# Kernel tuning notes

Hardware: AMD Instinct MI355X
Metric: run time of the kernel (lower is better)

Reference implementation:

```python
import jax, jax.numpy as jnp
import numpy as np

HEADS = 16

def setup_inputs() -> dict:
    key = jax.random.key(0)
    ks = jax.random.split(key, 8)
    S, B, D = 2048, 2, 1024
    scale = 0.02
    return {
        'query': jax.random.normal(ks[0], (S, B, D), jnp.float32),
        'key':   jax.random.normal(ks[1], (S, B, D), jnp.float32),
        'value': jax.random.normal(ks[2], (S, B, D), jnp.float32),
        'Wq': jax.random.normal(ks[3], (D, D), jnp.float32) * scale,
        'bq': jnp.zeros((D,), jnp.float32),
        'Wk': jax.random.normal(ks[4], (D, D), jnp.float32) * scale,
        'bk': jnp.zeros((D,), jnp.float32),
        'Wv': jax.random.normal(ks[5], (D, D), jnp.float32) * scale,
        'bv': jnp.zeros((D,), jnp.float32),
        'Wo': jax.random.normal(ks[6], (D, D), jnp.float32) * scale,
        'bo': jnp.zeros((D,), jnp.float32),
    }

def reference(query, key, value, Wq, bq, Wk, bk, Wv, bv, Wo, bo):
    S, B, D = query.shape
    h = HEADS
    dk = D // h
    # projections: nn.Linear stores weight [out, in] -> x @ W.T + b
    q = (query @ Wq.T + bq).reshape(S, B, h, dk)
    k = (key   @ Wk.T + bk).reshape(S, B, h, dk)
    v = (value @ Wv.T + bv).reshape(S, B, h, dk)
    # scores: [i, j, b, h]
    scores = jnp.einsum('ibhd,jbhd->ijbh', q, k) / jnp.sqrt(jnp.asarray(dk, q.dtype))
    # original uses nn.Softmax(dim=1) -> softmax over key axis j
    attn = jax.nn.softmax(scores, axis=1)
    x = jnp.einsum('ijbh,jbhd->ibhd', attn, v).reshape(S, B, D)
    return x @ Wo.T + bo
```

## Files before the change

kernel.cpp:

```cpp
#include <hip/hip_runtime.h>
#include <hip/hip_bf16.h>
#include <math.h>

#define S_LEN  2048
#define NBATCH 2
#define DMODEL 1024
#define NHEADS 16
#define HDIM   64
#define MROWS  (S_LEN*NBATCH)
#define NBH    (NBATCH*NHEADS)

#define QSCALE 0.1803368801111f
#define DEFER_THR 11.5f

typedef __attribute__((ext_vector_type(8))) short          bf16x8;
typedef __attribute__((ext_vector_type(4))) float          f32x4;
typedef __attribute__((ext_vector_type(8))) unsigned short u16x8;

__device__ __forceinline__ unsigned short f2bf(float x) {
    union { __hip_bfloat16 h; unsigned short u; } c;
    c.h = __float2bfloat16(x);
    return c.u;
}
__device__ __forceinline__ unsigned int cvtpk_bf16(float lo, float hi) {
    unsigned int r;
    asm("v_cvt_pk_bf16_f32 %0, %1, %2" : "=v"(r) : "v"(lo), "v"(hi));
    return r;
}

__global__ __launch_bounds__(256)
void cvt7(const float* __restrict__ s0, const float* __restrict__ s1,
          const float* __restrict__ s2, const float* __restrict__ s3,
          const float* __restrict__ s4, const float* __restrict__ s5,
          const float* __restrict__ s6,
          unsigned short* __restrict__ d0, unsigned short* __restrict__ d1,
          unsigned short* __restrict__ d2, unsigned short* __restrict__ d3,
          unsigned short* __restrict__ d4, unsigned short* __restrict__ d5,
          unsigned short* __restrict__ d6)
{
    const float* s; unsigned short* d; int n;
    switch (blockIdx.y) {
        case 0: s = s0; d = d0; n = MROWS*DMODEL;  break;
        case 1: s = s1; d = d1; n = MROWS*DMODEL;  break;
        case 2: s = s2; d = d2; n = MROWS*DMODEL;  break;
        case 3: s = s3; d = d3; n = DMODEL*DMODEL; break;
        case 4: s = s4; d = d4; n = DMODEL*DMODEL; break;
        case 5: s = s5; d = d5; n = DMODEL*DMODEL; break;
        default: s = s6; d = d6; n = DMODEL*DMODEL; break;
    }
    int i = (blockIdx.x*256 + threadIdx.x) * 8;
    if (i >= n) return;
    float4 a = *(const float4*)(s + i);
    float4 b = *(const float4*)(s + i + 4);
    u16x8 o;
    o[0] = f2bf(a.x); o[1] = f2bf(a.y); o[2] = f2bf(a.z); o[3] = f2bf(a.w);
    o[4] = f2bf(b.x); o[5] = f2bf(b.y); o[6] = f2bf(b.z); o[7] = f2bf(b.w);
    *(u16x8*)(d + i) = o;
}

#define GBM 128
#define GBK 32

template<int BN_T, bool TRANS>
__device__ __forceinline__ void gemm_core(
    const unsigned short* __restrict__ A,
    const unsigned short* __restrict__ W,
    const float* __restrict__ bias,
    float* __restrict__ Cf, unsigned short* __restrict__ Cb,
    int mode, float scale)
{
    constexpr int FN  = BN_T / 32;
    constexpr int BCW = BN_T / 64;
    __shared__ __align__(16) unsigned short As[GBM*GBK];
    __shared__ __align__(16) unsigned short Bs[BN_T*GBK];

    const int tid = threadIdx.x;
    const int l   = tid & 63;
    const int w   = tid >> 6;
    const int m0  = blockIdx.y * GBM;
    const int n0  = blockIdx.x * BN_T;
    const int wm  = (w >> 1) * 64;
    const int wn  = (w & 1) * (BN_T/2);

    f32x4 acc[4][FN];
    #pragma unroll
    for (int i = 0; i < 4; ++i)
        #pragma unroll
        for (int j = 0; j < FN; ++j)
            acc[i][j] = (f32x4){0.f, 0.f, 0.f, 0.f};

    const int srow = l >> 2;
    const int scol = (l & 3) * 8;

    for (int k0 = 0; k0 < DMODEL; k0 += GBK) {
        #pragma unroll
        for (int i = 0; i < 2; ++i) {
            int c = w*2 + i;
            const unsigned short* ga = A + (size_t)(m0 + c*16 + srow)*DMODEL + k0 + scol;
            __builtin_amdgcn_global_load_lds(
                (const __attribute__((address_space(1))) void*)ga,
                (__attribute__((address_space(3))) void*)(As + c*512), 16, 0, 0);
        }
        #pragma unroll
        for (int i = 0; i < BCW; ++i) {
            int c = w*BCW + i;
            const unsigned short* gb = W + (size_t)(n0 + c*16 + srow)*DMODEL + k0 + scol;
            __builtin_amdgcn_global_load_lds(
                (const __attribute__((address_space(1))) void*)gb,
                (__attribute__((address_space(3))) void*)(Bs + c*512), 16, 0, 0);
        }
        __syncthreads();

        bf16x8 af[4], bfr[FN];
        #pragma unroll
        for (int f = 0; f < 4; ++f)
            af[f]  = *(const bf16x8*)(As + (wm + f*16 + (l & 15))*GBK + (l >> 4)*8);
        #pragma unroll
        for (int f = 0; f < FN; ++f)
            bfr[f] = *(const bf16x8*)(Bs + (wn + f*16 + (l & 15))*GBK + (l >> 4)*8);
        #pragma unroll
        for (int i = 0; i < 4; ++i)
            #pragma unroll
            for (int j = 0; j < FN; ++j)
                acc[i][j] = __builtin_amdgcn_mfma_f32_16x16x32_bf16(af[i], bfr[j], acc[i][j], 0, 0, 0);
        __syncthreads();
    }

    const int col_l = l & 15;
    const int row_l = (l >> 4) * 4;

    if constexpr (TRANS) {
        if (mode == 2) {
            __shared__ __align__(16) unsigned short tileS[64][136];
            #pragma unroll
            for (int ph = 0; ph < 2; ++ph) {
                __syncthreads();
                if ((w >> 1) == ph) {
                    #pragma unroll
                    for (int j = 0; j < FN; ++j) {
                        int c = wn + j*16 + col_l;
                        float bv = bias[n0 + c];
                        #pragma unroll
                        for (int i = 0; i < 4; ++i)
                            #pragma unroll
                            for (int r = 0; r < 4; ++r)
                                tileS[i*16 + row_l + r][c] = f2bf((acc[i][j][r] + bv) * scale);
                    }
                }
                __syncthreads();
                const int sbase = (m0 + ph*64) >> 1;
                #pragma unroll
                for (int it = 0; it < 4; ++it) {
                    int idx = it*256 + tid;
                    int c    = idx >> 3;
                    int bb   = (idx >> 2) & 1;
                    int sl0  = (idx & 3) * 8;
                    int hh   = (n0 + c) >> 6;
                    int dd   = (n0 + c) & 63;
                    u16x8 ov;
                    #pragma unroll
                    for (int k2 = 0; k2 < 8; ++k2)
                        ov[k2] = tileS[2*(sl0 + k2) + bb][c];
                    *(u16x8*)(Cb + ((size_t)(bb*NHEADS + hh)*HDIM + dd)*S_LEN + sbase + sl0) = ov;
                }
            }
            return;
        }
    }

    #pragma unroll
    for (int j = 0; j < FN; ++j) {
        int col = n0 + wn + j*16 + col_l;
        float bv = bias[col];
        #pragma unroll
        for (int i = 0; i < 4; ++i) {
            int mbase = m0 + wm + i*16 + row_l;
            #pragma unroll
            for (int r = 0; r < 4; ++r) {
                int m = mbase + r;
                float vout = (acc[i][j][r] + bv) * scale;
                if (mode == 0) {
                    Cf[(size_t)m*DMODEL + col] = vout;
                } else {
                    int s = m >> 1, b = m & 1;
                    int h = col >> 6, d = col & 63;
                    Cb[((size_t)(b*NHEADS + h)*S_LEN + s)*HDIM + d] = f2bf(vout);
                }
            }
        }
    }
}

__global__ __launch_bounds__(256)
void gemm_qkv(const unsigned short* __restrict__ qb, const unsigned short* __restrict__ kb,
              const unsigned short* __restrict__ vb,
              const unsigned short* __restrict__ Wqb, const float* __restrict__ bq,
              const unsigned short* __restrict__ Wkb, const float* __restrict__ bk,
              const unsigned short* __restrict__ Wvb, const float* __restrict__ bv,
              unsigned short* __restrict__ qp, unsigned short* __restrict__ kp,
              unsigned short* __restrict__ vt)
{
    const int z = blockIdx.z;
    const unsigned short* A = (z==0) ? qb  : (z==1) ? kb  : vb;
    const unsigned short* W = (z==0) ? Wqb : (z==1) ? Wkb : Wvb;
    const float* bias       = (z==0) ? bq  : (z==1) ? bk  : bv;
    unsigned short* C       = (z==0) ? qp  : (z==1) ? kp  : vt;
    int   mode  = (z==2) ? 2 : 1;
    float scale = (z==0) ? QSCALE : 1.0f;
    gemm_core<128, true>(A, W, bias, nullptr, C, mode, scale);
}

__global__ __launch_bounds__(256)
void gemm_out(const unsigned short* __restrict__ A, const unsigned short* __restrict__ W,
              const float* __restrict__ bias, float* __restrict__ C)
{
    gemm_core<64, false>(A, W, bias, C, nullptr, 0, 1.0f);
}

#define QBLK  128
#define KVBLK 64
#define NT    (S_LEN/KVBLK)

__global__ __launch_bounds__(512)
void attn_mfma(const unsigned short* __restrict__ qp, const unsigned short* __restrict__ kp,
               const unsigned short* __restrict__ vt, unsigned short* __restrict__ x)
{
    __shared__ __align__(16) unsigned short Ks[2][KVBLK*HDIM];
    __shared__ __align__(16) unsigned short Vs[2][KVBLK*HDIM];
    __shared__ __align__(16) unsigned short Ps[8][16*KVBLK];

    const int tid = threadIdx.x;
    const int w   = tid >> 6;
    const int l   = tid & 63;
    const int g   = l >> 4;
    const int s16 = l & 15;
    const int q0  = blockIdx.x * QBLK;
    const int bh  = blockIdx.y;
    const int b   = bh >> 4;
    const int h   = bh & 15;
    const size_t base = (size_t)bh * S_LEN * HDIM;

    char* PsB = (char*)&Ps[w][0];

#define STAGE(buf_, kt_) do {                                                        \
    int row_ = tid >> 3;                                                             \
    int u_   = (tid & 7) ^ (row_ & 7);                                               \
    const unsigned short* gk_ = kp + base + (size_t)((kt_) + row_)*HDIM + u_*8;      \
    __builtin_amdgcn_global_load_lds(                                                \
        (const __attribute__((address_space(1))) void*)gk_,                          \
        (__attribute__((address_space(3))) void*)(Ks[buf_] + w*512), 16, 0, 0);      \
    const unsigned short* gv_ = vt + base + (size_t)row_*S_LEN + (kt_) + u_*8;       \
    __builtin_amdgcn_global_load_lds(                                                \
        (const __attribute__((address_space(1))) void*)gv_,                          \
        (__attribute__((address_space(3))) void*)(Vs[buf_] + w*512), 16, 0, 0);      \
} while (0)

#define ITER(buf_, t_) do {                                                          \
    __syncthreads();                                                                 \
    if ((t_) + 1 < NT) STAGE(buf_ ^ 1, ((t_) + 1)*KVBLK);                            \
    const char* KsB_ = (const char*)Ks[buf_];                                        \
    const char* VsB_ = (const char*)Vs[buf_];                                        \
    f32x4 sacc[4];                                                                   \
    _Pragma("unroll")                                                                \
    for (int mi = 0; mi < 4; ++mi) sacc[mi] = (f32x4){0.f, 0.f, 0.f, 0.f};           \
    __builtin_amdgcn_s_setprio(1);                                                   \
    _Pragma("unroll")                                                                \
    for (int ks = 0; ks < 2; ++ks) {                                                 \
        bf16x8 af[4];                                                                \
        _Pragma("unroll")                                                            \
        for (int mi = 0; mi < 4; ++mi) {                                             \
            int key  = mi*16 + s16;                                                  \
            int addr = ((key << 7) + (ks << 6) + (g << 4)) ^ ((key & 7) << 4);       \
            af[mi] = *(const bf16x8*)(KsB_ + addr);                                  \
        }                                                                            \
        _Pragma("unroll")                                                            \
        for (int mi = 0; mi < 4; ++mi)                                               \
            sacc[mi] = __builtin_amdgcn_mfma_f32_16x16x32_bf16(af[mi], qf[ks], sacc[mi], 0, 0, 0); \
    }                                                                                \
    __builtin_amdgcn_s_setprio(0);                                                   \
                          \
    float t0_ = fmaxf(fmaxf(sacc[0][0], sacc[0][1]), sacc[0][2]);                    \
    float t1_ = fmaxf(fmaxf(sacc[0][3], sacc[1][0]), sacc[1][1]);                    \
    float t2_ = fmaxf(fmaxf(sacc[1][2], sacc[1][3]), sacc[2][0]);                    \
    float t3_ = fmaxf(fmaxf(sacc[2][1], sacc[2][2]), sacc[2][3]);                    \
    float t4_ = fmaxf(fmaxf(sacc[3][0], sacc[3][1]), sacc[3][2]);                    \
    float tm_ = fmaxf(fmaxf(fmaxf(t0_, t1_), t2_), fmaxf(fmaxf(t3_, t4_), sacc[3][3])); \
    float mn_;                                                                       \
     \
    if (__all(tm_ <= run_m + DEFER_THR)) {                                           \
        mn_ = run_m;                                                                 \
    } else {                                                                         \
        float tr_ = fmaxf(tm_, __shfl_xor(tm_, 16));                                 \
        tr_ = fmaxf(tr_, __shfl_xor(tr_, 32));                                       \
        mn_ = fmaxf(run_m, tr_);                                                     \
        float al_ = exp2f(run_m - mn_);                                              \
        run_m = mn_;                                                                 \
        part_l *= al_;                                                               \
        float a0_ = __shfl(al_, 20*g + 0), a1_ = __shfl(al_, 20*g + 1);              \
        float a2_ = __shfl(al_, 20*g + 2), a3_ = __shfl(al_, 20*g + 3);              \
        _Pragma("unroll")                                                            \
        for (int nj = 0; nj < 4; ++nj) {                                             \
            oacc[nj][0] *= a0_; oacc[nj][1] *= a1_;                                  \
            oacc[nj][2] *= a2_; oacc[nj][3] *= a3_;                                  \
        }                                                                            \
    }                                                                                \
            \
    float ps_ = 0.f;                                                                 \
    _Pragma("unroll")                                                                \
    for (int mi = 0; mi < 4; ++mi) {                                                 \
        float p0_ = exp2f(sacc[mi][0] - mn_);                                        \
        float p1_ = exp2f(sacc[mi][1] - mn_);                                        \
        float p2_ = exp2f(sacc[mi][2] - mn_);                                        \
        float p3_ = exp2f(sacc[mi][3] - mn_);                                        \
        ps_ += (p0_ + p1_) + (p2_ + p3_);                                            \
        uint2 wv_; wv_.x = cvtpk_bf16(p0_, p1_); wv_.y = cvtpk_bf16(p2_, p3_);       \
        int addr = ((s16 << 7) + (mi << 5) + (g << 3)) ^ ((s16 & 7) << 4);           \
        *(uint2*)(PsB + addr) = wv_;                                                 \
    }                                                                                \
    part_l += ps_;                                                                   \
                                  \
    __builtin_amdgcn_s_setprio(1);                                                   \
    _Pragma("unroll")                                                                \
    for (int ks = 0; ks < 2; ++ks) {                                                 \
        int paddr = ((s16 << 7) + (ks << 6) + (g << 4)) ^ ((s16 & 7) << 4);          \
        bf16x8 pa = *(const bf16x8*)(PsB + paddr);                                   \
        _Pragma("unroll")                                                            \
        for (int nj = 0; nj < 4; ++nj) {                                             \
            int d    = nj*16 + s16;                                                  \
            int addr = ((d << 7) + (ks << 6) + (g << 4)) ^ ((d & 7) << 4);           \
            bf16x8 bv = *(const bf16x8*)(VsB_ + addr);                               \
            oacc[nj] = __builtin_amdgcn_mfma_f32_16x16x32_bf16(pa, bv, oacc[nj], 0, 0, 0); \
        }                                                                            \
    }                                                                                \
    __builtin_amdgcn_s_setprio(0);                                                   \
} while (0)

    bf16x8 qf[2];
    #pragma unroll
    for (int ks = 0; ks < 2; ++ks)
        qf[ks] = *(const bf16x8*)(qp + base + (size_t)(q0 + w*16 + s16)*HDIM + ks*32 + g*8);

    f32x4 oacc[4];
    #pragma unroll
    for (int nj = 0; nj < 4; ++nj) oacc[nj] = (f32x4){0.f, 0.f, 0.f, 0.f};
    float run_m  = -1e30f;
    float part_l = 0.f;

    STAGE(0, 0);

    for (int t = 0; t < NT; t += 2) {
        ITER(0, t);
        ITER(1, t + 1);
    }
#undef ITER
#undef STAGE

    float lt = part_l;
    lt += __shfl_xor(lt, 16);
    lt += __shfl_xor(lt, 32);
    #pragma unroll
    for (int r = 0; r < 4; ++r) {
        float rl  = __shfl(lt, 20*g + r);
        float inv = 1.f / rl;
        int row = q0 + w*16 + 4*g + r;
        #pragma unroll
        for (int nj = 0; nj < 4; ++nj) {
            int col = h*HDIM + nj*16 + s16;
            x[(size_t)(row*NBATCH + b)*DMODEL + col] = f2bf(oacc[nj][r] * inv);
        }
    }
}

extern "C" void kernel_launch(void* const* d_in, const int* in_sizes, int n_in,
                              void* d_out, int out_size, void* d_ws, size_t ws_size,
                              hipStream_t stream)
{
    const float* query = (const float*)d_in[0];
    const float* key_i = (const float*)d_in[1];
    const float* value = (const float*)d_in[2];
    const float* Wq = (const float*)d_in[3];
    const float* bq = (const float*)d_in[4];
    const float* Wk = (const float*)d_in[5];
    const float* bk = (const float*)d_in[6];
    const float* Wv = (const float*)d_in[7];
    const float* bv = (const float*)d_in[8];
    const float* Wo = (const float*)d_in[9];
    const float* bo = (const float*)d_in[10];
    float* out = (float*)d_out;

    char* ws = (char*)d_ws;
    unsigned short* qb  = (unsigned short*)(ws);
    unsigned short* kb2 = (unsigned short*)(ws + (size_t) 8*1024*1024);
    unsigned short* vb  = (unsigned short*)(ws + (size_t)16*1024*1024);
    unsigned short* Wqb = (unsigned short*)(ws + (size_t)24*1024*1024);
    unsigned short* Wkb = (unsigned short*)(ws + (size_t)26*1024*1024);
    unsigned short* Wvb = (unsigned short*)(ws + (size_t)28*1024*1024);
    unsigned short* Wob = (unsigned short*)(ws + (size_t)30*1024*1024);
    unsigned short* qp  = (unsigned short*)(ws + (size_t)32*1024*1024);
    unsigned short* kp  = (unsigned short*)(ws + (size_t)40*1024*1024);
    unsigned short* vt  = (unsigned short*)(ws + (size_t)48*1024*1024);
    unsigned short* xab = (unsigned short*)(ws + (size_t)56*1024*1024);

    dim3 gCvt(MROWS*DMODEL/(256*8), 7);
    cvt7<<<gCvt, 256, 0, stream>>>(query, key_i, value, Wq, Wk, Wv, Wo,
                                   qb, kb2, vb, Wqb, Wkb, Wvb, Wob);

    dim3 gQKV(DMODEL/128, MROWS/GBM, 3);
    gemm_qkv<<<gQKV, 256, 0, stream>>>(qb, kb2, vb,
                                       Wqb, bq, Wkb, bk, Wvb, bv,
                                       qp, kp, vt);

    dim3 gAttn(S_LEN/QBLK, NBH);
    attn_mfma<<<gAttn, 512, 0, stream>>>(qp, kp, vt, xab);

    dim3 gOut(DMODEL/64, MROWS/GBM);
    gemm_out<<<gOut, 256, 0, stream>>>(xab, Wob, bo, out);
}
```

Baseline: 253.2 us.

## Vectorize GEMM epilogue stores via swapped MFMA operands and split V projection kernel

Swaps the MFMA operand order for the Q/K and output GEMMs so each lane holds four consecutive output columns. This enables float4 and packed bf16x4 stores in the epilogue instead of scalar strided stores. The V projection with its transposed layout moves into its own kernel with a compile-time mode, which removes runtime mode branching. The conversion kernel also uses packed bf16 conversion. The cost is one more kernel launch, and the QKV grid is split into two launches that can no longer share a single wave of blocks.

```diff
diff --git a/kernel.cpp b/kernel.cpp
--- a/kernel.cpp
+++ b/kernel.cpp
@@ -52,22 +52,24 @@
     if (i >= n) return;
     float4 a = *(const float4*)(s + i);
     float4 b = *(const float4*)(s + i + 4);
-    u16x8 o;
-    o[0] = f2bf(a.x); o[1] = f2bf(a.y); o[2] = f2bf(a.z); o[3] = f2bf(a.w);
-    o[4] = f2bf(b.x); o[5] = f2bf(b.y); o[6] = f2bf(b.z); o[7] = f2bf(b.w);
-    *(u16x8*)(d + i) = o;
+    uint4 o;
+    o.x = cvtpk_bf16(a.x, a.y);
+    o.y = cvtpk_bf16(a.z, a.w);
+    o.z = cvtpk_bf16(b.x, b.y);
+    o.w = cvtpk_bf16(b.z, b.w);
+    *(uint4*)(d + i) = o;
 }
 
 #define GBM 128
 #define GBK 32
 
-template<int BN_T, bool TRANS>
+template<int BN_T, int MODE>
 __device__ __forceinline__ void gemm_core(
     const unsigned short* __restrict__ A,
     const unsigned short* __restrict__ W,
     const float* __restrict__ bias,
     float* __restrict__ Cf, unsigned short* __restrict__ Cb,
-    int mode, float scale)
+    float scale)
 {
     constexpr int FN  = BN_T / 32;
     constexpr int BCW = BN_T / 64;
@@ -121,70 +123,72 @@
         #pragma unroll
         for (int i = 0; i < 4; ++i)
             #pragma unroll
-            for (int j = 0; j < FN; ++j)
-                acc[i][j] = __builtin_amdgcn_mfma_f32_16x16x32_bf16(af[i], bfr[j], acc[i][j], 0, 0, 0);
+            for (int j = 0; j < FN; ++j) {
+                if constexpr (MODE == 2)
+                    acc[i][j] = __builtin_amdgcn_mfma_f32_16x16x32_bf16(af[i], bfr[j], acc[i][j], 0, 0, 0);
+                else
+                    acc[i][j] = __builtin_amdgcn_mfma_f32_16x16x32_bf16(bfr[j], af[i], acc[i][j], 0, 0, 0);
+            }
         __syncthreads();
     }
 
     const int col_l = l & 15;
     const int row_l = (l >> 4) * 4;
 
-    if constexpr (TRANS) {
-        if (mode == 2) {
-            __shared__ __align__(16) unsigned short tileS[64][136];
-            #pragma unroll
-            for (int ph = 0; ph < 2; ++ph) {
-                __syncthreads();
-                if ((w >> 1) == ph) {
+    if constexpr (MODE == 2) {
+        __shared__ __align__(16) unsigned short tileS[64][136];
+        #pragma unroll
+        for (int ph = 0; ph < 2; ++ph) {
+            __syncthreads();
+            if ((w >> 1) == ph) {
+                #pragma unroll
+                for (int j = 0; j < FN; ++j) {
+                    int c = wn + j*16 + col_l;
+                    float bv = bias[n0 + c];
                     #pragma unroll
-                    for (int j = 0; j < FN; ++j) {
-                        int c = wn + j*16 + col_l;
-                        float bv = bias[n0 + c];
+                    for (int i = 0; i < 4; ++i)
                         #pragma unroll
-                        for (int i = 0; i < 4; ++i)
-                            #pragma unroll
-                            for (int r = 0; r < 4; ++r)
-                                tileS[i*16 + row_l + r][c] = f2bf((acc[i][j][r] + bv) * scale);
-                    }
-                }
-                __syncthreads();
-                const int sbase = (m0 + ph*64) >> 1;
-                #pragma unroll
-                for (int it = 0; it < 4; ++it) {
-                    int idx = it*256 + tid;
-                    int c    = idx >> 3;
-                    int bb   = (idx >> 2) & 1;
-                    int sl0  = (idx & 3) * 8;
-                    int hh   = (n0 + c) >> 6;
-                    int dd   = (n0 + c) & 63;
-                    u16x8 ov;
-                    #pragma unroll
-                    for (int k2 = 0; k2 < 8; ++k2)
-                        ov[k2] = tileS[2*(sl0 + k2) + bb][c];
-                    *(u16x8*)(Cb + ((size_t)(bb*NHEADS + hh)*HDIM + dd)*S_LEN + sbase + sl0) = ov;
+                        for (int r = 0; r < 4; ++r)
+                            tileS[i*16 + row_l + r][c] = f2bf((acc[i][j][r] + bv) * scale);
                 }
             }
-            return;
+            __syncthreads();
+            const int sbase = (m0 + ph*64) >> 1;
+            #pragma unroll
+            for (int it = 0; it < 4; ++it) {
+                int idx = it*256 + tid;
+                int c    = idx >> 3;
+                int bb   = (idx >> 2) & 1;
+                int sl0  = (idx & 3) * 8;
+                int hh   = (n0 + c) >> 6;
+                int dd   = (n0 + c) & 63;
+                u16x8 ov;
+                #pragma unroll
+                for (int k2 = 0; k2 < 8; ++k2)
+                    ov[k2] = tileS[2*(sl0 + k2) + bb][c];
+                *(u16x8*)(Cb + ((size_t)(bb*NHEADS + hh)*HDIM + dd)*S_LEN + sbase + sl0) = ov;
+            }
         }
-    }
-
-    #pragma unroll
-    for (int j = 0; j < FN; ++j) {
-        int col = n0 + wn + j*16 + col_l;
-        float bv = bias[col];
-        #pragma unroll
-        for (int i = 0; i < 4; ++i) {
-            int mbase = m0 + wm + i*16 + row_l;
+        return;
+    } else {
+        #pragma unroll
+        for (int j = 0; j < FN; ++j) {
+            const int nb = n0 + wn + j*16 + row_l;
+            float4 bi = *(const float4*)(bias + nb);
             #pragma unroll
-            for (int r = 0; r < 4; ++r) {
-                int m = mbase + r;
-                float vout = (acc[i][j][r] + bv) * scale;
-                if (mode == 0) {
-                    Cf[(size_t)m*DMODEL + col] = vout;
+            for (int i = 0; i < 4; ++i) {
+                const int m = m0 + wm + i*16 + col_l;
+                f32x4 a = acc[i][j];
+                if constexpr (MODE == 0) {
+                    float4 ov = make_float4(a[0]+bi.x, a[1]+bi.y, a[2]+bi.z, a[3]+bi.w);
+                    *(float4*)(Cf + (size_t)m*DMODEL + nb) = ov;
                 } else {
-                    int s = m >> 1, b = m & 1;
-                    int h = col >> 6, d = col & 63;
-                    Cb[((size_t)(b*NHEADS + h)*S_LEN + s)*HDIM + d] = f2bf(vout);
+                    const int s = m >> 1, b = m & 1;
+                    const int h = nb >> 6, d = nb & 63;
+                    uint2 pk;
+                    pk.x = cvtpk_bf16((a[0]+bi.x)*scale, (a[1]+bi.y)*scale);
+                    pk.y = cvtpk_bf16((a[2]+bi.z)*scale, (a[3]+bi.w)*scale);
+                    *(uint2*)(Cb + ((size_t)(b*NHEADS + h)*S_LEN + s)*HDIM + d) = pk;
                 }
             }
         }
@@ -192,29 +196,32 @@
 }
 
 __global__ __launch_bounds__(256)
-void gemm_qkv(const unsigned short* __restrict__ qb, const unsigned short* __restrict__ kb,
-              const unsigned short* __restrict__ vb,
-              const unsigned short* __restrict__ Wqb, const float* __restrict__ bq,
-              const unsigned short* __restrict__ Wkb, const float* __restrict__ bk,
-              const unsigned short* __restrict__ Wvb, const float* __restrict__ bv,
-              unsigned short* __restrict__ qp, unsigned short* __restrict__ kp,
-              unsigned short* __restrict__ vt)
+void gemm_qk(const unsigned short* __restrict__ qb, const unsigned short* __restrict__ kb,
+             const unsigned short* __restrict__ Wqb, const float* __restrict__ bq,
+             const unsigned short* __restrict__ Wkb, const float* __restrict__ bk,
+             unsigned short* __restrict__ qp, unsigned short* __restrict__ kp)
 {
     const int z = blockIdx.z;
-    const unsigned short* A = (z==0) ? qb  : (z==1) ? kb  : vb;
-    const unsigned short* W = (z==0) ? Wqb : (z==1) ? Wkb : Wvb;
-    const float* bias       = (z==0) ? bq  : (z==1) ? bk  : bv;
-    unsigned short* C       = (z==0) ? qp  : (z==1) ? kp  : vt;
-    int   mode  = (z==2) ? 2 : 1;
-    float scale = (z==0) ? QSCALE : 1.0f;
-    gemm_core<128, true>(A, W, bias, nullptr, C, mode, scale);
+    const unsigned short* A = (z==0) ? qb  : kb;
+    const unsigned short* W = (z==0) ? Wqb : Wkb;
+    const float* bias       = (z==0) ? bq  : bk;
+    unsigned short* C       = (z==0) ? qp  : kp;
+    float scale             = (z==0) ? QSCALE : 1.0f;
+    gemm_core<128, 1>(A, W, bias, nullptr, C, scale);
+}
+
+__global__ __launch_bounds__(256)
+void gemm_v(const unsigned short* __restrict__ vb, const unsigned short* __restrict__ Wvb,
+            const float* __restrict__ bv, unsigned short* __restrict__ vt)
+{
+    gemm_core<128, 2>(vb, Wvb, bv, nullptr, vt, 1.0f);
 }
 
 __global__ __launch_bounds__(256)
 void gemm_out(const unsigned short* __restrict__ A, const unsigned short* __restrict__ W,
               const float* __restrict__ bias, float* __restrict__ C)
 {
-    gemm_core<64, false>(A, W, bias, C, nullptr, 0, 1.0f);
+    gemm_core<64, 0>(A, W, bias, C, nullptr, 1.0f);
 }
 
 #define QBLK  128
@@ -278,7 +285,6 @@
             sacc[mi] = __builtin_amdgcn_mfma_f32_16x16x32_bf16(af[mi], qf[ks], sacc[mi], 0, 0, 0); \
     }                                                                                \
     __builtin_amdgcn_s_setprio(0);                                                   \
-                          \
     float t0_ = fmaxf(fmaxf(sacc[0][0], sacc[0][1]), sacc[0][2]);                    \
     float t1_ = fmaxf(fmaxf(sacc[0][3], sacc[1][0]), sacc[1][1]);                    \
     float t2_ = fmaxf(fmaxf(sacc[1][2], sacc[1][3]), sacc[2][0]);                    \
@@ -286,7 +292,6 @@
     float t4_ = fmaxf(fmaxf(sacc[3][0], sacc[3][1]), sacc[3][2]);                    \
     float tm_ = fmaxf(fmaxf(fmaxf(t0_, t1_), t2_), fmaxf(fmaxf(t3_, t4_), sacc[3][3])); \
     float mn_;                                                                       \
-     \
     if (__all(tm_ <= run_m + DEFER_THR)) {                                           \
         mn_ = run_m;                                                                 \
     } else {                                                                         \
@@ -304,7 +309,6 @@
             oacc[nj][2] *= a2_; oacc[nj][3] *= a3_;                                  \
         }                                                                            \
     }                                                                                \
-            \
     float ps_ = 0.f;                                                                 \
     _Pragma("unroll")                                                                \
     for (int mi = 0; mi < 4; ++mi) {                                                 \
@@ -318,7 +322,6 @@
         *(uint2*)(PsB + addr) = wv_;                                                 \
     }                                                                                \
     part_l += ps_;                                                                   \
-                                  \
     __builtin_amdgcn_s_setprio(1);                                                   \
     _Pragma("unroll")                                                                \
     for (int ks = 0; ks < 2; ++ks) {                                                 \
@@ -405,10 +408,11 @@
     cvt7<<<gCvt, 256, 0, stream>>>(query, key_i, value, Wq, Wk, Wv, Wo,
                                    qb, kb2, vb, Wqb, Wkb, Wvb, Wob);
 
-    dim3 gQKV(DMODEL/128, MROWS/GBM, 3);
-    gemm_qkv<<<gQKV, 256, 0, stream>>>(qb, kb2, vb,
-                                       Wqb, bq, Wkb, bk, Wvb, bv,
-                                       qp, kp, vt);
+    dim3 gQK(DMODEL/128, MROWS/GBM, 2);
+    gemm_qk<<<gQK, 256, 0, stream>>>(qb, kb2, Wqb, bq, Wkb, bk, qp, kp);
+
+    dim3 gV(DMODEL/128, MROWS/GBM);
+    gemm_v<<<gV, 256, 0, stream>>>(vb, Wvb, bv, vt);
 
     dim3 gAttn(S_LEN/QBLK, NBH);
     attn_mfma<<<gAttn, 512, 0, stream>>>(qp, kp, vt, xab);
```

After: 261.6 us. 1.03x slower.
